# Optimization experiments

Measured on AMD Instinct MI355X. Metric: run time of the kernel, lower is better.

Reference implementation:

```python
import jax, jax.numpy as jnp
import numpy as np
import math

BS, A, M, C = 16, 8400, 64, 80
TOPK, ALPHA, BETA, EPS = 10, 0.5, 6.0, 1e-9
BG_IDX = C
IMG = 640.0


def setup_inputs() -> dict:
    key = jax.random.key(0)
    ks = jax.random.split(key, 6)
    pd_scores = jax.random.uniform(ks[0], (BS, A, C), jnp.float32)  # post-sigmoid scores
    anc_points = jax.random.uniform(ks[1], (A, 2), jnp.float32) * IMG
    pwh = jax.random.uniform(ks[2], (BS, A, 2), jnp.float32) * 120.0 + 8.0
    pd_bboxes = jnp.concatenate([anc_points[None] - pwh / 2, anc_points[None] + pwh / 2], -1)
    gxy = jax.random.uniform(ks[3], (BS, M, 2), jnp.float32) * (IMG - 140.0)
    gwh = jax.random.uniform(ks[4], (BS, M, 2), jnp.float32) * 120.0 + 8.0
    gt_bboxes = jnp.concatenate([gxy, gxy + gwh], -1)  # valid xyxy
    gt_labels = jax.random.randint(ks[5], (BS, M, 1), 0, C)
    mask_gt = jnp.ones((BS, M, 1), bool)
    return dict(pd_scores=pd_scores, pd_bboxes=pd_bboxes, anc_points=anc_points,
                gt_labels=gt_labels, gt_bboxes=gt_bboxes, mask_gt=mask_gt)


def pairwise_ciou(b1, b2, eps=1e-7):
    # b1: (bs, M, 4) gt xyxy ; b2: (bs, A, 4) pred xyxy -> (bs, M, A) CIoU
    b1x1, b1y1, b1x2, b1y2 = jnp.split(b1, 4, -1)               # (bs, M, 1)
    c2x1, c2y1, c2x2, c2y2 = jnp.split(b2, 4, -1)               # (bs, A, 1)
    T = lambda t: t.swapaxes(-1, -2)                             # -> (bs, 1, A)
    b2x1, b2y1, b2x2, b2y2 = T(c2x1), T(c2y1), T(c2x2), T(c2y2)
    w1, h1 = b1x2 - b1x1, b1y2 - b1y1
    w2, h2 = b2x2 - b2x1, b2y2 - b2y1
    inter = (jnp.clip(jnp.minimum(b1x2, b2x2) - jnp.maximum(b1x1, b2x1), 0)
             * jnp.clip(jnp.minimum(b1y2, b2y2) - jnp.maximum(b1y1, b2y1), 0))
    union = w1 * h1 + w2 * h2 - inter + eps
    iou = inter / union
    cw = jnp.maximum(b1x2, b2x2) - jnp.minimum(b1x1, b2x1)
    ch = jnp.maximum(b1y2, b2y2) - jnp.minimum(b1y1, b2y1)
    c2 = cw ** 2 + ch ** 2 + eps
    rho2 = (((b2x1 + b2x2) - (b1x1 + b1x2)) ** 2 + ((b2y1 + b2y2) - (b1y1 + b1y2)) ** 2) / 4
    v = (4 / math.pi ** 2) * (jnp.arctan(w1 / (h1 + eps)) - jnp.arctan(w2 / (h2 + eps))) ** 2
    alpha = jax.lax.stop_gradient(v / (v - iou + (1 + eps)))
    return iou - (rho2 / c2 + v * alpha)


def _assign(pd_scores, pd_bboxes, anc_points, gt_labels, gt_bboxes, mask_gt):
    bs, n_anchors, nc = pd_scores.shape
    n_max = gt_labels.shape[1]
    gt_l = gt_labels[..., 0]                                      # (bs, M)
    mgt = mask_gt[..., 0]                                         # (bs, M) bool

    # --- candidates whose center lies inside a GT box ---
    lt, rb = gt_bboxes[:, :, None, :2], gt_bboxes[:, :, None, 2:]
    deltas = jnp.concatenate([anc_points[None, None] - lt, rb - anc_points[None, None]], -1)
    mask_in_gts = deltas.min(-1) > EPS                            # (bs, M, A)
    valid = mask_in_gts & mgt[:, :, None]

    # --- alignment metric: score^alpha * CIoU^beta ---
    overlaps = jnp.where(valid, jnp.clip(pairwise_ciou(gt_bboxes, pd_bboxes), 0), 0.0)
    lbl = jnp.clip(gt_l, 0, nc - 1)
    b_idx = jnp.arange(bs)[:, None, None]
    a_idx = jnp.arange(n_anchors)[None, None, :]
    bbox_scores = pd_scores[b_idx, a_idx, lbl[:, :, None]]        # (bs, M, A)
    align = jnp.where(valid, bbox_scores ** ALPHA * overlaps ** BETA, 0.0)

    # --- per-GT top-k candidate selection ---
    _, topk_idxs = jax.lax.top_k(align, TOPK)                     # (bs, M, TOPK)
    valid_k = jnp.broadcast_to(mgt[:, :, None], topk_idxs.shape)
    topk_idxs = jnp.where(valid_k, topk_idxs, 0)
    m_idx = jnp.arange(n_max)[None, :, None]
    counts = jnp.zeros((bs, n_max, n_anchors), align.dtype).at[
        b_idx, m_idx, topk_idxs].add(valid_k.astype(align.dtype))
    mask_topk = jnp.where(counts > 1, 0.0, counts)                # drop duplicate hits
    mask_pos = mask_topk * mask_in_gts.astype(align.dtype) * mgt[:, :, None].astype(align.dtype)

    # --- resolve anchors assigned to multiple GTs by highest overlap ---
    fg = mask_pos.sum(1)                                          # (bs, A)
    mask_multi = fg[:, None, :] > 1
    is_max = jax.nn.one_hot(overlaps.argmax(1), n_max, dtype=align.dtype).transpose(0, 2, 1)
    mask_pos = jnp.where(mask_multi, is_max, mask_pos)
    fg = mask_pos.sum(1)
    target_gt_idx = mask_pos.argmax(1)                            # (bs, A)

    # --- gather targets ---
    flat_idx = target_gt_idx + jnp.arange(bs)[:, None] * n_max
    target_labels = gt_l.reshape(-1)[flat_idx]                    # (bs, A)
    target_bboxes = gt_bboxes.reshape(-1, 4)[flat_idx]            # (bs, A, 4)
    fg_bool = fg > 0
    target_scores = jax.nn.one_hot(jnp.clip(target_labels, 0, None), nc, dtype=pd_scores.dtype)
    target_scores = jnp.where(fg_bool[..., None], target_scores, 0.0)

    # --- normalize scores by aligned metric ---
    align = align * mask_pos
    pos_align = align.max(-1, keepdims=True)                      # (bs, M, 1)
    pos_ov = (overlaps * mask_pos).max(-1, keepdims=True)
    norm = (align * pos_ov / (pos_align + EPS)).max(1)[..., None]  # (bs, A, 1)
    target_scores = target_scores * norm

    target_labels = jnp.where(fg_bool, target_labels, BG_IDX)
    return target_labels, target_bboxes, target_scores, fg_bool, target_gt_idx


def reference(pd_scores, pd_bboxes, anc_points, gt_labels, gt_bboxes, mask_gt):
    return _assign(pd_scores, pd_bboxes, anc_points, gt_labels, gt_bboxes, mask_gt)
```

## Files before the change

### kernel.cpp

```cpp
#include <hip/hip_runtime.h>


#define BSZ   16
#define NA    8400
#define NM    64
#define NC    80
#define TOPKN 10
#define EPS9  1e-9f
#define EPS7  1e-7f
#define NCHUNK 33
#define SEGCAP 64
#define LCMAX  (NCHUNK*SEGCAP)

#define O_LBL 0
#define O_BB  (BSZ*NA)
#define O_SC  (O_BB + BSZ*NA*4)
#define O_FG  (O_SC + BSZ*NA*NC)
#define O_TG  (O_FG + BSZ*NA)

#define W_PA   0
#define W_POV  (W_PA + BSZ*NM)
#define W_AL   (W_POV + BSZ*NM)
#define W_SEL  (W_AL + BSZ*NA)
#define W_CNT2 (W_SEL + BSZ*NM*TOPKN)
#define W_CAND (W_CNT2 + BSZ*NM*NCHUNK)

typedef unsigned long long ull;

__device__ __forceinline__ float ciou_f(float gx1,float gy1,float gx2,float gy2,
                                        float px1,float py1,float px2,float py2){
  float w1=gx2-gx1, h1=gy2-gy1, w2=px2-px1, h2=py2-py1;
  float iw=fmaxf(fminf(gx2,px2)-fmaxf(gx1,px1),0.f);
  float ih=fmaxf(fminf(gy2,py2)-fmaxf(gy1,py1),0.f);
  float inter=iw*ih;
  float uni=w1*h1+w2*h2-inter+EPS7;
  float iou=inter/uni;
  float cw=fmaxf(gx2,px2)-fminf(gx1,px1);
  float ch=fmaxf(gy2,py2)-fminf(gy1,py1);
  float c2=cw*cw+ch*ch+EPS7;
  float dx=(px1+px2)-(gx1+gx2);
  float dy=(py1+py2)-(gy1+gy2);
  float rho2=(dx*dx+dy*dy)*0.25f;
  float da=atanf(w1/(h1+EPS7))-atanf(w2/(h2+EPS7));
  float v=0.40528473456935108577f*da*da;
  float alpha=v/(v-iou+(1.f+EPS7));
  return iou-(rho2/c2+v*alpha);
}

__global__ __launch_bounds__(256) void k_scan(
    const float* __restrict__ pd_scores,
    const float* __restrict__ pd_bboxes,
    const float* __restrict__ anc,
    const int*  __restrict__ gt_labels,
    const float* __restrict__ gt_bboxes,
    int* __restrict__ cnt2,
    ull* __restrict__ cand){
  const int chunk = blockIdx.x, b = blockIdx.y, tid = threadIdx.x;
  __shared__ float4 gbox[NM];
  __shared__ int    glab[NM];
  __shared__ int    cl[NM];
  if (tid < NM){
    gbox[tid] = ((const float4*)gt_bboxes)[b*NM + tid];
    int l = gt_labels[b*NM + tid];
    glab[tid] = l < 0 ? 0 : (l > NC-1 ? NC-1 : l);
    cl[tid] = 0;
  }
  __syncthreads();
  const int a = chunk*256 + tid;
  if (a < NA){
    const float2 ap = ((const float2*)anc)[a];
    ull mk = 0;
    #pragma unroll 8
    for (int m = 0; m < NM; m++){
      float4 g = gbox[m];
      float dmin = fminf(fminf(ap.x-g.x, ap.y-g.y), fminf(g.z-ap.x, g.w-ap.y));
      if (dmin > EPS9) mk |= (1ull << m);
    }
    if (mk){
      const float4 p = ((const float4*)pd_bboxes)[b*NA + a];
      const float* srow = pd_scores + ((size_t)b*NA + a)*NC;
      while (mk){
        int m = __builtin_ctzll(mk);
        mk &= mk - 1;
        float4 g = gbox[m];
        float ov = fmaxf(ciou_f(g.x,g.y,g.z,g.w, p.x,p.y,p.z,p.w), 0.f);
        if (ov > 0.f){
          float s  = srow[glab[m]];
          float o2 = ov*ov;
          float al = sqrtf(s)*(o2*o2*o2);
          int slot = atomicAdd(&cl[m], 1);
          if (slot < SEGCAP)
            cand[(size_t)((b*NM + m)*NCHUNK + chunk)*SEGCAP + slot] =
                ((ull)__float_as_uint(al) << 32) | (unsigned)(NA - a);
        }
      }
    }
  }
  __syncthreads();
  if (tid < NM) cnt2[(b*NM + tid)*NCHUNK + chunk] = cl[tid];
}

__global__ __launch_bounds__(64) void k_top(
    const int* __restrict__ cnt2,
    const ull* __restrict__ cand,
    const float* __restrict__ anc,
    const float* __restrict__ gt_bboxes,
    const float* __restrict__ pd_scores,
    const float* __restrict__ pd_bboxes,
    const int*  __restrict__ gt_labels,
    unsigned* __restrict__ sel_out,
    unsigned* __restrict__ pa_g,
    unsigned* __restrict__ pov_g){
  const int bm = blockIdx.x, b = bm >> 6;
  const int lane = threadIdx.x;
  __shared__ ull lc[LCMAX + TOPKN];
  __shared__ ull zk[TOPKN];
  const float4 g = ((const float4*)gt_bboxes)[bm];

  int c = (lane < NCHUNK) ? cnt2[bm*NCHUNK + lane] : 0;
  bool ovf_any = __any(c > SEGCAP);
  int v = c;
  #pragma unroll
  for (int off = 1; off < 64; off <<= 1){
    int u = __shfl_up(v, off, 64);
    if (lane >= off) v += u;
  }
  const int base = v - c;
  const int n = __shfl(v, 63, 64);

  if (lane < TOPKN) zk[lane] = 0;
  {
    int h = 0;
    for (int ab = 0; ab < NA && h < TOPKN; ab += 64){
      int a = ab + lane;
      bool nonpos = false;
      if (a < NA){
        float2 ap = ((const float2*)anc)[a];
        float dmin = fminf(fminf(ap.x-g.x, ap.y-g.y), fminf(g.z-ap.x, g.w-ap.y));
        bool pos = false;
        if (dmin > EPS9){
          float4 p = ((const float4*)pd_bboxes)[b*NA + a];
          pos = ciou_f(g.x,g.y,g.z,g.w, p.x,p.y,p.z,p.w) > 0.f;
        }
        nonpos = !pos;
      }
      ull mask = __ballot(nonpos);
      if (nonpos){
        int r = h + __popcll(mask & ((1ull << lane) - 1ull));
        if (r < TOPKN) zk[r] = (ull)(unsigned)(NA - a);
      }
      h += __popcll(mask);
    }
  }
  __syncthreads();

  ull sel[TOPKN];
  if (!ovf_any){
    if (lane < NCHUNK){
      const ull* seg = cand + (size_t)(bm*NCHUNK + lane)*SEGCAP;
      for (int i = 0; i < c; i++) lc[base + i] = seg[i];
    }
    __syncthreads();
    #pragma unroll
    for (int t = 0; t < TOPKN; t++){
      ull best = 0;
      const int L = n + TOPKN;
      for (int i = lane; i < L; i += 64){
        ull k = (i < n) ? lc[i] : zk[i - n];
        bool skip = false;
        #pragma unroll
        for (int j = 0; j < TOPKN; j++)
          if (j < t) skip |= (k == sel[j]);
        if (!skip && k > best) best = k;
      }
      #pragma unroll
      for (int off = 32; off; off >>= 1){
        ull o = __shfl_xor(best, off, 64);
        if (o > best) best = o;
      }
      sel[t] = best;
    }
  } else {
    int lbl = gt_labels[bm]; lbl = lbl < 0 ? 0 : (lbl > NC-1 ? NC-1 : lbl);
    #pragma unroll
    for (int t = 0; t < TOPKN; t++){
      ull best = 0;
      for (int a = lane; a < NA; a += 64){
        float2 ap = ((const float2*)anc)[a];
        float dmin = fminf(fminf(ap.x-g.x, ap.y-g.y), fminf(g.z-ap.x, g.w-ap.y));
        float ov = 0.f;
        if (dmin > EPS9){
          float4 p = ((const float4*)pd_bboxes)[b*NA + a];
          ov = fmaxf(ciou_f(g.x,g.y,g.z,g.w, p.x,p.y,p.z,p.w), 0.f);
        }
        ull key;
        if (ov > 0.f){
          float s = pd_scores[((size_t)b*NA + a)*NC + lbl];
          float o2 = ov*ov;
          key = ((ull)__float_as_uint(sqrtf(s)*(o2*o2*o2)) << 32)
              | (unsigned)(NA - a);
        } else key = (ull)(unsigned)(NA - a);
        bool skip = false;
        #pragma unroll
        for (int j = 0; j < TOPKN; j++)
          if (j < t) skip |= (key == sel[j]);
        if (!skip && key > best) best = key;
      }
      #pragma unroll
      for (int off = 32; off; off >>= 1){
        ull o = __shfl_xor(best, off, 64);
        if (o > best) best = o;
      }
      sel[t] = best;
    }
  }

  if (lane < TOPKN){
    ull key = 0;
    #pragma unroll
    for (int t = 0; t < TOPKN; t++) if (lane == t) key = sel[t];
    unsigned outv = 0;
    if (key){
      int a = NA - (int)(key & 0xFFFFFFFFull);
      bool ok = true;
      if ((key >> 32) == 0){
        float2 ap = ((const float2*)anc)[a];
        float dmin = fminf(fminf(ap.x-g.x, ap.y-g.y), fminf(g.z-ap.x, g.w-ap.y));
        ok = dmin > EPS9;
      }
      if (ok) outv = (unsigned)(NA - a);
    }
    sel_out[bm*TOPKN + lane] = outv;
  }
  if (lane == 0){ pa_g[bm] = 0u; pov_g[bm] = 0u; }
}

__global__ __launch_bounds__(256) void k_resolve(
    const float* __restrict__ pd_scores,
    const float* __restrict__ pd_bboxes,
    const float* __restrict__ anc,
    const int*  __restrict__ gt_labels,
    const float* __restrict__ gt_bboxes,
    const unsigned* __restrict__ sel_out,
    float* __restrict__ al_g,
    unsigned* __restrict__ pa_g,
    unsigned* __restrict__ pov_g,
    float* out){
  const int chunk = blockIdx.x, b = blockIdx.y, tid = threadIdx.x;
  __shared__ float4 gbox[NM];
  __shared__ int    glab[NM];
  __shared__ int    fg_l[256];
  __shared__ int    tgt_l[256];
  if (tid < NM){
    gbox[tid] = ((const float4*)gt_bboxes)[b*NM + tid];
    glab[tid] = gt_labels[b*NM + tid];
  }
  fg_l[tid] = 0;
  __syncthreads();
  const int a0 = chunk*256;
  for (int e = tid; e < NM*TOPKN; e += 256){
    unsigned v = sel_out[b*NM*TOPKN + e];
    if (v){
      int a = NA - (int)v;
      unsigned la = (unsigned)(a - a0);
      if (la < 256u){
        atomicAdd(&fg_l[la], 1);
        tgt_l[la] = e / TOPKN;
      }
    }
  }
  __syncthreads();
  const int a = a0 + tid;
  if (a >= NA) return;
  const int idx = b*NA + a;
  const int c = fg_l[tid];
  const bool fg = c > 0;
  int tgt = 0;
  float ov_t = 0.f;
  if (c == 1){
    tgt = tgt_l[tid];
    const float4 p = ((const float4*)pd_bboxes)[idx];
    float4 g = gbox[tgt];
    ov_t = fmaxf(ciou_f(g.x,g.y,g.z,g.w, p.x,p.y,p.z,p.w), 0.f);
  } else if (c > 1){
    const float2 ap = ((const float2*)anc)[a];
    const float4 p = ((const float4*)pd_bboxes)[idx];
    float bv = 0.f;
    for (int m = 0; m < NM; m++){
      float4 g = gbox[m];
      float dmin = fminf(fminf(ap.x-g.x, ap.y-g.y), fminf(g.z-ap.x, g.w-ap.y));
      if (dmin > EPS9){
        float v = fmaxf(ciou_f(g.x,g.y,g.z,g.w, p.x,p.y,p.z,p.w), 0.f);
        if (v > bv){ bv = v; tgt = m; }
      }
    }
    ov_t = bv;
  }
  const int lraw = glab[tgt];
  out[O_LBL + idx] = fg ? (float)lraw : 80.0f;
  ((float4*)(out + O_BB))[idx] = gbox[tgt];
  out[O_FG + idx] = fg ? 1.f : 0.f;
  out[O_TG + idx] = (float)tgt;
  float al = 0.f;
  if (fg){
    int l = lraw < 0 ? 0 : (lraw > NC-1 ? NC-1 : lraw);
    float s = pd_scores[(size_t)idx*NC + l];
    float o2 = ov_t*ov_t;
    al = sqrtf(s)*(o2*o2*o2);
    int bm = b*NM + tgt;
    atomicMax(&pa_g[bm],  __float_as_uint(al));
    atomicMax(&pov_g[bm], __float_as_uint(ov_t));
  }
  al_g[idx] = al;
}

__global__ void k_scores(const float* out_ro,
                         const float* __restrict__ align_as,
                         const unsigned int* __restrict__ pa_bits,
                         const unsigned int* __restrict__ pov_bits,
                         const int* __restrict__ gt_labels,
                         float* out){
  int e = blockIdx.x*256 + threadIdx.x;
  if (e >= BSZ*NA*(NC/4)) return;
  int ba = e / (NC/4);
  int q  = e - ba*(NC/4);
  float4 z = {0.f,0.f,0.f,0.f};
  if (out_ro[O_FG + ba] > 0.f){
    int b = ba / NA;
    int tgt = (int)out_ro[O_TG + ba];
    int bm = b*NM + tgt;
    int lc = gt_labels[bm]; if (lc < 0) lc = 0;
    if ((lc >> 2) == q){
      float pa  = __uint_as_float(pa_bits[bm]);
      float pov = __uint_as_float(pov_bits[bm]);
      float norm = (align_as[ba] * pov) / (pa + EPS9);
      int base = q*4;
      z.x = (lc==base  ) ? norm : 0.f;
      z.y = (lc==base+1) ? norm : 0.f;
      z.z = (lc==base+2) ? norm : 0.f;
      z.w = (lc==base+3) ? norm : 0.f;
    }
  }
  ((float4*)(out + O_SC))[e] = z;
}

extern "C" void kernel_launch(void* const* d_in, const int* in_sizes, int n_in,
                              void* d_out, int out_size, void* d_ws, size_t ws_size,
                              hipStream_t stream){
  const float* pd_scores = (const float*)d_in[0];
  const float* pd_bboxes = (const float*)d_in[1];
  const float* anc       = (const float*)d_in[2];
  const int*   gt_labels = (const int*)d_in[3];
  const float* gt_bboxes = (const float*)d_in[4];

  float* ws = (float*)d_ws;
  unsigned* pa      = (unsigned*)(ws + W_PA);
  unsigned* povb    = (unsigned*)(ws + W_POV);
  float*    al_as   = ws + W_AL;
  unsigned* sel     = (unsigned*)(ws + W_SEL);
  int*      cnt2    = (int*)(ws + W_CNT2);
  ull*      cand    = (ull*)(ws + W_CAND);
  float*    out     = (float*)d_out;

  k_scan<<<dim3(NCHUNK, BSZ), 256, 0, stream>>>(pd_scores, pd_bboxes, anc,
                                                gt_labels, gt_bboxes, cnt2, cand);
  k_top<<<BSZ*NM, 64, 0, stream>>>(cnt2, cand, anc, gt_bboxes, pd_scores,
                                   pd_bboxes, gt_labels, sel, pa, povb);
  k_resolve<<<dim3(NCHUNK, BSZ), 256, 0, stream>>>(pd_scores, pd_bboxes, anc,
                                                   gt_labels, gt_bboxes, sel,
                                                   al_as, pa, povb, out);
  k_scores<<<(BSZ*NA*(NC/4)+255)/256, 256, 0, stream>>>(out, al_as, pa, povb,
                                                        gt_labels, out);
}
```

Measured before the change: 49.75 us.

## Fuse candidate scan and top-k into one per-GT kernel

Replaces the per-anchor-chunk scan kernel and the per-GT top-k kernel with a single kernel launched per (batch, GT). Each 256-thread block scans all anchors for its GT and collects positive candidates in shared memory, then one wavefront runs the top-k selection. This drops a launch and the global candidate buffer round trip. It also computes the non-positive fallback keys only when fewer than k positive keys exist. In exchange, every block reads anchor points and predicted boxes for all 8400 anchors, so box and score traffic per GT rises, and 3 of the 4 waves sit idle during selection.

```diff
diff --git a/kernel.cpp b/kernel.cpp
--- a/kernel.cpp
+++ b/kernel.cpp
@@ -8,9 +8,7 @@
 #define TOPKN 10
 #define EPS9  1e-9f
 #define EPS7  1e-7f
-#define NCHUNK 33
-#define SEGCAP 64
-#define LCMAX  (NCHUNK*SEGCAP)
+#define CAP   2048
 
 #define O_LBL 0
 #define O_BB  (BSZ*NA)
@@ -22,8 +20,6 @@
 #define W_POV  (W_PA + BSZ*NM)
 #define W_AL   (W_POV + BSZ*NM)
 #define W_SEL  (W_AL + BSZ*NA)
-#define W_CNT2 (W_SEL + BSZ*NM*TOPKN)
-#define W_CAND (W_CNT2 + BSZ*NM*NCHUNK)
 
 typedef unsigned long long ull;
 
@@ -47,192 +43,177 @@
   return iou-(rho2/c2+v*alpha);
 }
 
-__global__ __launch_bounds__(256) void k_scan(
+__global__ __launch_bounds__(256) void k_fuse(
     const float* __restrict__ pd_scores,
     const float* __restrict__ pd_bboxes,
     const float* __restrict__ anc,
     const int*  __restrict__ gt_labels,
     const float* __restrict__ gt_bboxes,
-    int* __restrict__ cnt2,
-    ull* __restrict__ cand){
-  const int chunk = blockIdx.x, b = blockIdx.y, tid = threadIdx.x;
-  __shared__ float4 gbox[NM];
-  __shared__ int    glab[NM];
-  __shared__ int    cl[NM];
-  if (tid < NM){
-    gbox[tid] = ((const float4*)gt_bboxes)[b*NM + tid];
-    int l = gt_labels[b*NM + tid];
-    glab[tid] = l < 0 ? 0 : (l > NC-1 ? NC-1 : l);
-    cl[tid] = 0;
-  }
-  __syncthreads();
-  const int a = chunk*256 + tid;
-  if (a < NA){
-    const float2 ap = ((const float2*)anc)[a];
-    ull mk = 0;
-    #pragma unroll 8
-    for (int m = 0; m < NM; m++){
-      float4 g = gbox[m];
-      float dmin = fminf(fminf(ap.x-g.x, ap.y-g.y), fminf(g.z-ap.x, g.w-ap.y));
-      if (dmin > EPS9) mk |= (1ull << m);
-    }
-    if (mk){
-      const float4 p = ((const float4*)pd_bboxes)[b*NA + a];
-      const float* srow = pd_scores + ((size_t)b*NA + a)*NC;
-      while (mk){
-        int m = __builtin_ctzll(mk);
-        mk &= mk - 1;
-        float4 g = gbox[m];
-        float ov = fmaxf(ciou_f(g.x,g.y,g.z,g.w, p.x,p.y,p.z,p.w), 0.f);
-        if (ov > 0.f){
-          float s  = srow[glab[m]];
-          float o2 = ov*ov;
-          float al = sqrtf(s)*(o2*o2*o2);
-          int slot = atomicAdd(&cl[m], 1);
-          if (slot < SEGCAP)
-            cand[(size_t)((b*NM + m)*NCHUNK + chunk)*SEGCAP + slot] =
-                ((ull)__float_as_uint(al) << 32) | (unsigned)(NA - a);
-        }
-      }
-    }
-  }
-  __syncthreads();
-  if (tid < NM) cnt2[(b*NM + tid)*NCHUNK + chunk] = cl[tid];
-}
-
-__global__ __launch_bounds__(64) void k_top(
-    const int* __restrict__ cnt2,
-    const ull* __restrict__ cand,
-    const float* __restrict__ anc,
-    const float* __restrict__ gt_bboxes,
-    const float* __restrict__ pd_scores,
-    const float* __restrict__ pd_bboxes,
-    const int*  __restrict__ gt_labels,
     unsigned* __restrict__ sel_out,
     unsigned* __restrict__ pa_g,
     unsigned* __restrict__ pov_g){
   const int bm = blockIdx.x, b = bm >> 6;
-  const int lane = threadIdx.x;
-  __shared__ ull lc[LCMAX + TOPKN];
+  const int tid = threadIdx.x;
+  __shared__ ull lc[CAP + TOPKN];
   __shared__ ull zk[TOPKN];
+  __shared__ int s_n;
+
   const float4 g = ((const float4*)gt_bboxes)[bm];
-
-  int c = (lane < NCHUNK) ? cnt2[bm*NCHUNK + lane] : 0;
-  bool ovf_any = __any(c > SEGCAP);
-  int v = c;
-  #pragma unroll
-  for (int off = 1; off < 64; off <<= 1){
-    int u = __shfl_up(v, off, 64);
-    if (lane >= off) v += u;
-  }
-  const int base = v - c;
-  const int n = __shfl(v, 63, 64);
-
-  if (lane < TOPKN) zk[lane] = 0;
-  {
-    int h = 0;
-    for (int ab = 0; ab < NA && h < TOPKN; ab += 64){
-      int a = ab + lane;
-      bool nonpos = false;
-      if (a < NA){
-        float2 ap = ((const float2*)anc)[a];
-        float dmin = fminf(fminf(ap.x-g.x, ap.y-g.y), fminf(g.z-ap.x, g.w-ap.y));
-        bool pos = false;
-        if (dmin > EPS9){
-          float4 p = ((const float4*)pd_bboxes)[b*NA + a];
-          pos = ciou_f(g.x,g.y,g.z,g.w, p.x,p.y,p.z,p.w) > 0.f;
-        }
-        nonpos = !pos;
-      }
-      ull mask = __ballot(nonpos);
-      if (nonpos){
-        int r = h + __popcll(mask & ((1ull << lane) - 1ull));
-        if (r < TOPKN) zk[r] = (ull)(unsigned)(NA - a);
-      }
-      h += __popcll(mask);
-    }
-  }
+  int lbl = gt_labels[bm]; lbl = lbl < 0 ? 0 : (lbl > NC-1 ? NC-1 : lbl);
+  const float* srow = pd_scores + (size_t)b*NA*NC + lbl;
+
+  if (tid == 0) s_n = 0;
   __syncthreads();
 
-  ull sel[TOPKN];
-  if (!ovf_any){
-    if (lane < NCHUNK){
-      const ull* seg = cand + (size_t)(bm*NCHUNK + lane)*SEGCAP;
-      for (int i = 0; i < c; i++) lc[base + i] = seg[i];
-    }
-    __syncthreads();
-    #pragma unroll
-    for (int t = 0; t < TOPKN; t++){
-      ull best = 0;
-      const int L = n + TOPKN;
-      for (int i = lane; i < L; i += 64){
-        ull k = (i < n) ? lc[i] : zk[i - n];
-        bool skip = false;
+  for (int k = 0; k < 33; k++){
+    int a = k*256 + tid;
+    if (a < NA){
+      const float2 ap = ((const float2*)anc)[a];
+      float dmin = fminf(fminf(ap.x-g.x, ap.y-g.y), fminf(g.z-ap.x, g.w-ap.y));
+      if (dmin > EPS9){
+        const float4 p = ((const float4*)pd_bboxes)[b*NA + a];
+        float ov = fmaxf(ciou_f(g.x,g.y,g.z,g.w, p.x,p.y,p.z,p.w), 0.f);
+        if (ov > 0.f){
+          float s  = srow[(size_t)a*NC];
+          float o2 = ov*ov;
+          float al = sqrtf(s)*(o2*o2*o2);
+          int slot = atomicAdd(&s_n, 1);
+          if (slot < CAP)
+            lc[slot] = ((ull)__float_as_uint(al) << 32) | (unsigned)(NA - a);
+        }
+      }
+    }
+  }
+  __syncthreads();
+  const int n = s_n;
+
+  if (tid < 64){
+    const int lane = tid;
+    ull sel[TOPKN];
+
+    if (n <= CAP){
+      #pragma unroll
+      for (int t = 0; t < TOPKN; t++){
+        ull best = 0;
+        for (int i = lane; i < n; i += 64){
+          ull k = lc[i];
+          bool skip = false;
+          #pragma unroll
+          for (int j = 0; j < TOPKN; j++)
+            if (j < t) skip |= (k == sel[j]);
+          if (!skip && k > best) best = k;
+        }
         #pragma unroll
-        for (int j = 0; j < TOPKN; j++)
-          if (j < t) skip |= (k == sel[j]);
-        if (!skip && k > best) best = k;
-      }
+        for (int off = 32; off; off >>= 1){
+          ull o = __shfl_xor(best, off, 64);
+          if (o > best) best = o;
+        }
+        sel[t] = best;
+      }
+
+      bool need = (n < TOPKN);
       #pragma unroll
-      for (int off = 32; off; off >>= 1){
-        ull o = __shfl_xor(best, off, 64);
-        if (o > best) best = o;
-      }
-      sel[t] = best;
-    }
-  } else {
-    int lbl = gt_labels[bm]; lbl = lbl < 0 ? 0 : (lbl > NC-1 ? NC-1 : lbl);
-    #pragma unroll
-    for (int t = 0; t < TOPKN; t++){
-      ull best = 0;
-      for (int a = lane; a < NA; a += 64){
-        float2 ap = ((const float2*)anc)[a];
-        float dmin = fminf(fminf(ap.x-g.x, ap.y-g.y), fminf(g.z-ap.x, g.w-ap.y));
-        float ov = 0.f;
-        if (dmin > EPS9){
-          float4 p = ((const float4*)pd_bboxes)[b*NA + a];
-          ov = fmaxf(ciou_f(g.x,g.y,g.z,g.w, p.x,p.y,p.z,p.w), 0.f);
-        }
-        ull key;
-        if (ov > 0.f){
-          float s = pd_scores[((size_t)b*NA + a)*NC + lbl];
-          float o2 = ov*ov;
-          key = ((ull)__float_as_uint(sqrtf(s)*(o2*o2*o2)) << 32)
-              | (unsigned)(NA - a);
-        } else key = (ull)(unsigned)(NA - a);
-        bool skip = false;
+      for (int t = 0; t < TOPKN; t++) if ((sel[t] >> 32) == 0) need = true;
+
+      if (need){
+        if (lane < TOPKN) zk[lane] = 0;
+        int h = 0;
+        for (int ab = 0; ab < NA && h < TOPKN; ab += 64){
+          int a = ab + lane;
+          bool nonpos = false;
+          if (a < NA){
+            float2 ap = ((const float2*)anc)[a];
+            float dmin = fminf(fminf(ap.x-g.x, ap.y-g.y),
+                               fminf(g.z-ap.x, g.w-ap.y));
+            bool pos = false;
+            if (dmin > EPS9){
+              float4 p = ((const float4*)pd_bboxes)[b*NA + a];
+              pos = ciou_f(g.x,g.y,g.z,g.w, p.x,p.y,p.z,p.w) > 0.f;
+            }
+            nonpos = !pos;
+          }
+          ull mask = __ballot(nonpos);
+          if (nonpos){
+            int r = h + __popcll(mask & ((1ull << lane) - 1ull));
+            if (r < TOPKN) zk[r] = (ull)(unsigned)(NA - a);
+          }
+          h += __popcll(mask);
+        }
+        if (lane < TOPKN) lc[n + lane] = zk[lane];
+        const int L = n + TOPKN;
         #pragma unroll
-        for (int j = 0; j < TOPKN; j++)
-          if (j < t) skip |= (key == sel[j]);
-        if (!skip && key > best) best = key;
-      }
+        for (int t = 0; t < TOPKN; t++){
+          ull best = 0;
+          for (int i = lane; i < L; i += 64){
+            ull k = lc[i];
+            bool skip = false;
+            #pragma unroll
+            for (int j = 0; j < TOPKN; j++)
+              if (j < t) skip |= (k == sel[j]);
+            if (!skip && k > best) best = k;
+          }
+          #pragma unroll
+          for (int off = 32; off; off >>= 1){
+            ull o = __shfl_xor(best, off, 64);
+            if (o > best) best = o;
+          }
+          sel[t] = best;
+        }
+      }
+    } else {
       #pragma unroll
-      for (int off = 32; off; off >>= 1){
-        ull o = __shfl_xor(best, off, 64);
-        if (o > best) best = o;
-      }
-      sel[t] = best;
-    }
-  }
-
-  if (lane < TOPKN){
-    ull key = 0;
-    #pragma unroll
-    for (int t = 0; t < TOPKN; t++) if (lane == t) key = sel[t];
-    unsigned outv = 0;
-    if (key){
-      int a = NA - (int)(key & 0xFFFFFFFFull);
-      bool ok = true;
-      if ((key >> 32) == 0){
-        float2 ap = ((const float2*)anc)[a];
-        float dmin = fminf(fminf(ap.x-g.x, ap.y-g.y), fminf(g.z-ap.x, g.w-ap.y));
-        ok = dmin > EPS9;
-      }
-      if (ok) outv = (unsigned)(NA - a);
-    }
-    sel_out[bm*TOPKN + lane] = outv;
-  }
-  if (lane == 0){ pa_g[bm] = 0u; pov_g[bm] = 0u; }
+      for (int t = 0; t < TOPKN; t++){
+        ull best = 0;
+        for (int a = lane; a < NA; a += 64){
+          float2 ap = ((const float2*)anc)[a];
+          float dmin = fminf(fminf(ap.x-g.x, ap.y-g.y),
+                             fminf(g.z-ap.x, g.w-ap.y));
+          float ov = 0.f;
+          if (dmin > EPS9){
+            float4 p = ((const float4*)pd_bboxes)[b*NA + a];
+            ov = fmaxf(ciou_f(g.x,g.y,g.z,g.w, p.x,p.y,p.z,p.w), 0.f);
+          }
+          ull key;
+          if (ov > 0.f){
+            float o2 = ov*ov;
+            key = ((ull)__float_as_uint(sqrtf(srow[(size_t)a*NC])*(o2*o2*o2)) << 32)
+                | (unsigned)(NA - a);
+          } else key = (ull)(unsigned)(NA - a);
+          bool skip = false;
+          #pragma unroll
+          for (int j = 0; j < TOPKN; j++)
+            if (j < t) skip |= (key == sel[j]);
+          if (!skip && key > best) best = key;
+        }
+        #pragma unroll
+        for (int off = 32; off; off >>= 1){
+          ull o = __shfl_xor(best, off, 64);
+          if (o > best) best = o;
+        }
+        sel[t] = best;
+      }
+    }
+
+    if (lane < TOPKN){
+      ull key = 0;
+      #pragma unroll
+      for (int t = 0; t < TOPKN; t++) if (lane == t) key = sel[t];
+      unsigned outv = 0;
+      if (key){
+        int a = NA - (int)(key & 0xFFFFFFFFull);
+        bool inside = true;
+        if ((key >> 32) == 0){
+          float2 ap = ((const float2*)anc)[a];
+          float dmin = fminf(fminf(ap.x-g.x, ap.y-g.y),
+                             fminf(g.z-ap.x, g.w-ap.y));
+          inside = dmin > EPS9;
+        }
+        if (inside) outv = (unsigned)(NA - a);
+      }
+      sel_out[bm*TOPKN + lane] = outv;
+    }
+    if (lane == 0){ pa_g[bm] = 0u; pov_g[bm] = 0u; }
+  }
 }
 
 __global__ __launch_bounds__(256) void k_resolve(
@@ -354,21 +335,17 @@
   const float* gt_bboxes = (const float*)d_in[4];
 
   float* ws = (float*)d_ws;
-  unsigned* pa      = (unsigned*)(ws + W_PA);
-  unsigned* povb    = (unsigned*)(ws + W_POV);
-  float*    al_as   = ws + W_AL;
-  unsigned* sel     = (unsigned*)(ws + W_SEL);
-  int*      cnt2    = (int*)(ws + W_CNT2);
-  ull*      cand    = (ull*)(ws + W_CAND);
-  float*    out     = (float*)d_out;
-
-  k_scan<<<dim3(NCHUNK, BSZ), 256, 0, stream>>>(pd_scores, pd_bboxes, anc,
-                                                gt_labels, gt_bboxes, cnt2, cand);
-  k_top<<<BSZ*NM, 64, 0, stream>>>(cnt2, cand, anc, gt_bboxes, pd_scores,
-                                   pd_bboxes, gt_labels, sel, pa, povb);
-  k_resolve<<<dim3(NCHUNK, BSZ), 256, 0, stream>>>(pd_scores, pd_bboxes, anc,
-                                                   gt_labels, gt_bboxes, sel,
-                                                   al_as, pa, povb, out);
+  unsigned* pa    = (unsigned*)(ws + W_PA);
+  unsigned* povb  = (unsigned*)(ws + W_POV);
+  float*    al_as = ws + W_AL;
+  unsigned* sel   = (unsigned*)(ws + W_SEL);
+  float*    out   = (float*)d_out;
+
+  k_fuse<<<BSZ*NM, 256, 0, stream>>>(pd_scores, pd_bboxes, anc, gt_labels,
+                                     gt_bboxes, sel, pa, povb);
+  k_resolve<<<dim3(33, BSZ), 256, 0, stream>>>(pd_scores, pd_bboxes, anc,
+                                               gt_labels, gt_bboxes, sel,
+                                               al_as, pa, povb, out);
   k_scores<<<(BSZ*NA*(NC/4)+255)/256, 256, 0, stream>>>(out, al_as, pa, povb,
                                                         gt_labels, out);
 }
```

New measurement: 73.73 us. 48.2% more time.
